# Kernel optimization log

Hardware: AMD Instinct MI355X
Metric: run time of the kernel (lower is better)

## Reference

```python
import jax, jax.numpy as jnp
import numpy as np

K = 4096            # ca3_memory_slots
C = 2048            # ca3_code_dim
B = 8192            # query batch (episodes)
MAX_ITERS = 8       # cfg.pseudoinverse_iterations (spiking window T=8)
TOL = 1e-4          # cfg.convergence_tolerance
ALPHA_CLAMP = 5e-4  # torch.clamp(exp(log_scale), max=5e-4)


def setup_inputs() -> dict:
    key = jax.random.key(0)
    k1, k2, k3 = jax.random.split(key, 3)
    query = jax.random.normal(k1, (B, C), dtype=jnp.float32)
    # buffer init: torch.randn(K, C) * 0.01
    memory_mean = jax.random.normal(k2, (K, C), dtype=jnp.float32) * 0.01
    # nn.Parameter(torch.tensor(pseudoinverse_alpha_init)) -> scalar
    ben_israel_log_scale = jnp.float32(-0.5)
    return {"query": query, "memory_mean": memory_mean,
            "ben_israel_log_scale": ben_israel_log_scale}


def _ben_israel_pinv(A, log_scale):
    """Ben-Israel-Cohen iteration with masked early stopping (fixed trip count)."""
    A_fro_sq = jnp.sum(A * A)
    alpha = (1.0 / (A_fro_sq + 1e-8)) * jnp.minimum(jnp.exp(log_scale), ALPHA_CLAMP)
    pinv = alpha * A.T                       # (C, K)
    residual = jnp.array(jnp.inf, dtype=A.dtype)
    done = jnp.array(False)
    for _ in range(MAX_ITERS):
        pinv_new = 2.0 * pinv - pinv @ (A @ pinv)        # (C,K)
        recon = A @ (pinv_new @ A)                       # (K,C)
        res_new = jnp.linalg.norm(recon - A)             # Frobenius
        pinv = jnp.where(done, pinv, pinv_new)
        residual = jnp.where(done, residual, res_new)
        done = done | (res_new < TOL)
    return pinv, residual


def reference(query, memory_mean, ben_israel_log_scale):
    A = memory_mean                                      # (K, C)
    A_pinv, residual = _ben_israel_pinv(A, ben_israel_log_scale)  # (C, K)
    w = query @ A_pinv                                   # (B, K) addressing weights
    retrieved = w @ A                                    # (B, C) pattern completion
    return retrieved
```

## Files before the change

### kernel.cpp

```cpp
#include <hip/hip_runtime.h>
#include <hip/hip_bf16.h>
#include <cstdint>
#include <cstddef>


#define K_DIM 4096
#define C_DIM 2048
#define B_DIM 8192
#define SPLITK 4
#define KCHUNK (K_DIM / SPLITK)

typedef __bf16 bf16x8 __attribute__((ext_vector_type(8)));
typedef float f32x4 __attribute__((ext_vector_type(4)));

#define VMCNT(n) asm volatile("s_waitcnt vmcnt(" #n ")" ::: "memory")
#define LGKMCNT0 asm volatile("s_waitcnt lgkmcnt(0)" ::: "memory")
#define SBAR __builtin_amdgcn_s_barrier()

__device__ __forceinline__ void async_load16(const void* g, void* l) {
  __builtin_amdgcn_global_load_lds(
      (const __attribute__((address_space(1))) void*)g,
      (__attribute__((address_space(3))) void*)l, 16, 0, 0);
}

__global__ __launch_bounds__(256) void prep_kernel(
    const float* __restrict__ A, __hip_bfloat16* __restrict__ At,
    const float* __restrict__ q, __hip_bfloat16* __restrict__ qb,
    float* __restrict__ wsf) {
  const int b = blockIdx.x;
  const int t = threadIdx.x;
  if (b < 2048) {
    __shared__ __align__(16) __hip_bfloat16 Ts[64 * 68];
    const int c0 = (b & 31) * 64;
    const int k0 = (b >> 5) * 64;
    const int c_l = t & 63;
    const int kq = t >> 6;
#pragma unroll
    for (int i = 0; i < 4; ++i) {
      int k_l = i * 16 + kq * 4;
      union { __hip_bfloat16 h[4]; uint2 u; } pk;
#pragma unroll
      for (int j = 0; j < 4; ++j)
        pk.h[j] = __float2bfloat16(A[(size_t)(k0 + k_l + j) * C_DIM + c0 + c_l]);
      *(uint2*)(Ts + c_l * 68 + k_l) = pk.u;
    }
    __syncthreads();
    const int c = t >> 2;
    const int seg = t & 3;
    const __hip_bfloat16* src = Ts + c * 68 + seg * 16;
    union { uint2 d[2]; uint4 qv; } o0, o1;
    o0.d[0] = *(const uint2*)(src + 0);
    o0.d[1] = *(const uint2*)(src + 4);
    o1.d[0] = *(const uint2*)(src + 8);
    o1.d[1] = *(const uint2*)(src + 12);
    __hip_bfloat16* dst = At + (size_t)(c0 + c) * K_DIM + k0 + seg * 16;
    *(uint4*)(dst + 0) = o0.qv;
    *(uint4*)(dst + 8) = o1.qv;
  } else {
    if (b == 2048 && t == 0) wsf[4] = 0.0f;
    const int n4 = B_DIM * C_DIM / 4;
    int tid = (b - 2048) * 256 + t;
    for (int i = tid; i < n4; i += 1024 * 256) {
      float4 v = ((const float4*)q)[i];
      __hip_bfloat16 o[4] = {__float2bfloat16(v.x), __float2bfloat16(v.y),
                             __float2bfloat16(v.z), __float2bfloat16(v.w)};
      *(uint2*)(qb + 4 * (size_t)i) = *(const uint2*)o;
    }
  }
}

__global__ __launch_bounds__(256, 4) void gemm_m(
    const __hip_bfloat16* __restrict__ At, float* __restrict__ P) {
  constexpr int BK = 64;
  constexpr int NT = KCHUNK / BK;
  __shared__ __align__(16) __hip_bfloat16 As[128 * BK];
  __shared__ __align__(16) __hip_bfloat16 Bs[128 * BK];
  const int bid = blockIdx.x;
  const int sw = (bid & 7) * 128 + (bid >> 3);
  const int z = sw >> 8;
  const int r = sw & 255;
  const int tn_i = r >> 4;
  const int tm_i = r & 15;
  const int tid = threadIdx.x;
  const int wave = tid >> 6, lane = tid & 63;
  const int tile_m = tm_i * 128, tile_n = tn_i * 128;
  const int kstart = z * KCHUNK;
  const int wm = (wave >> 1) * 64, wn = (wave & 1) * 64;
  const int lr = lane >> 3, lcl = (lane & 7) ^ lr;
  const __hip_bfloat16* aB =
      At + (size_t)(tile_m + wave * 32 + lr) * K_DIM + kstart + lcl * 8;
  const __hip_bfloat16* bB =
      At + (size_t)(tile_n + wave * 32 + lr) * K_DIM + kstart + lcl * 8;
  const int l15 = lane & 15, lg = lane >> 4, l7 = lane & 7;
  f32x4 acc[4][4] = {};

  for (int t = 0; t < NT; ++t) {
#pragma unroll
    for (int c = 0; c < 4; ++c) {
      async_load16(aB + (size_t)(c * 8) * K_DIM + (size_t)t * BK,
                   &As[(wave * 32 + c * 8) * BK]);
      async_load16(bB + (size_t)(c * 8) * K_DIM + (size_t)t * BK,
                   &Bs[(wave * 32 + c * 8) * BK]);
    }
    __syncthreads();
#pragma unroll
    for (int kh = 0; kh < 2; ++kh) {
      bf16x8 a[4], bb[4];
#pragma unroll
      for (int f = 0; f < 4; ++f) {
        a[f]  = *(const bf16x8*)&As[(wm + f * 16 + l15) * BK +
                                    (((kh * 4 + lg) ^ l7) * 8)];
        bb[f] = *(const bf16x8*)&Bs[(wn + f * 16 + l15) * BK +
                                    (((kh * 4 + lg) ^ l7) * 8)];
      }
      __builtin_amdgcn_s_setprio(1);
#pragma unroll
      for (int f = 0; f < 4; ++f)
#pragma unroll
        for (int j = 0; j < 4; ++j)
          acc[f][j] = __builtin_amdgcn_mfma_f32_16x16x32_bf16(
              a[f], bb[j], acc[f][j], 0, 0, 0);
      __builtin_amdgcn_s_setprio(0);
    }
    __syncthreads();
  }

  float* Pz = P + (size_t)z * C_DIM * C_DIM;
#pragma unroll
  for (int f = 0; f < 4; ++f) {
    const int gm = tile_m + wm + f * 16 + lg * 4;
#pragma unroll
    for (int j = 0; j < 4; ++j) {
      const int gn = tile_n + wn + j * 16 + l15;
#pragma unroll
      for (int r2 = 0; r2 < 4; ++r2)
        Pz[(size_t)(gm + r2) * C_DIM + gn] = acc[f][j][r2];
    }
  }
}

__global__ __launch_bounds__(256) void reduce4_kernel(
    const float* __restrict__ P, __hip_bfloat16* __restrict__ Mb,
    float* __restrict__ wsf) {
  const size_t CC = (size_t)C_DIM * C_DIM;
  const int n4 = (int)(CC / 4);
  int tid = blockIdx.x * blockDim.x + threadIdx.x;
  int stride = gridDim.x * blockDim.x;
  float tsum = 0.0f;
  bool hit = false;
  for (int i = tid; i < n4; i += stride) {
    float4 a = ((const float4*)P)[i];
#pragma unroll
    for (int z = 1; z < SPLITK; ++z) {
      float4 b = *(const float4*)(P + z * CC + (size_t)i * 4);
      a.x += b.x; a.y += b.y; a.z += b.z; a.w += b.w;
    }
    __hip_bfloat16 o[4] = {__float2bfloat16(a.x), __float2bfloat16(a.y),
                           __float2bfloat16(a.z), __float2bfloat16(a.w)};
    *(uint2*)(Mb + 4 * (size_t)i) = *(const uint2*)o;
    const int e0 = 4 * i;
    const int g = e0 >> 11;
    const int d = g * (C_DIM + 1);
    if (d >= e0 && d < e0 + 4) {
      const float av[4] = {a.x, a.y, a.z, a.w};
      tsum += av[d - e0];
      hit = true;
    }
  }
  if (hit) atomicAdd(wsf + 4, tsum);
}

__global__ __launch_bounds__(512, 2) void gemm_qm(
    const __hip_bfloat16* __restrict__ Ab, const __hip_bfloat16* __restrict__ Bb,
    float* __restrict__ Fp, const float* __restrict__ ls,
    const float* __restrict__ wsf) {
  constexpr int BK = 64;
  constexpr int NT = C_DIM / BK;
  __shared__ __align__(16) __hip_bfloat16 As[2][256 * BK];
  __shared__ __align__(16) __hip_bfloat16 Bs[2][256 * BK];
  const int bid = blockIdx.x;
  const int sw = (bid & 7) * 32 + (bid >> 3);
  const int tn_i = sw & 7;
  const int tm_i = sw >> 3;
  const int tid = threadIdx.x;
  const int wave = tid >> 6, lane = tid & 63;
  const int tile_m = tm_i * 256, tile_n = tn_i * 256;
  const int wm = (wave >> 2) * 128, wn = (wave & 3) * 64;
  const int lr = lane >> 3, lcl = (lane & 7) ^ lr;
  const __hip_bfloat16* aBase =
      Ab + (size_t)(tile_m + wave * 16 + lr) * C_DIM + lcl * 8;
  const __hip_bfloat16* bBase =
      Bb + (size_t)(tile_n + wave * 16 + lr) * C_DIM + lcl * 8;
  const int l15 = lane & 15, lg = lane >> 4, l7 = lane & 7;

  auto stA = [&](int buf, int h, int t) {
    const __hip_bfloat16* s = aBase + (size_t)(h * 128) * C_DIM + (size_t)t * BK;
    __hip_bfloat16* d = &As[buf][(h * 128 + wave * 16) * BK];
    async_load16(s, d);
    async_load16(s + (size_t)8 * C_DIM, d + 8 * BK);
  };
  auto stB = [&](int buf, int h, int t) {
    const __hip_bfloat16* s = bBase + (size_t)(h * 128) * C_DIM + (size_t)t * BK;
    __hip_bfloat16* d = &Bs[buf][(h * 128 + wave * 16) * BK];
    async_load16(s, d);
    async_load16(s + (size_t)8 * C_DIM, d + 8 * BK);
  };

  f32x4 acc[8][4] = {};

  stA(0, 0, 0); stA(0, 1, 0);
  stB(0, 0, 0); stB(0, 1, 0);
  stB(1, 0, 1); stB(1, 1, 1);
  VMCNT(4);
  SBAR;

  for (int t = 0; t < NT; ++t) {
    const int buf = t & 1;
    bf16x8 breg[4][2];
#pragma unroll
    for (int q = 0; q < 4; ++q) {
      bf16x8 af[2][2];
#pragma unroll
      for (int f = 0; f < 2; ++f)
#pragma unroll
        for (int s = 0; s < 2; ++s)
          af[f][s] = *(const bf16x8*)&As[buf][(wm + q * 32 + f * 16 + l15) * BK +
                                             ((((s << 2) | lg) ^ l7) << 3)];
      if (q == 0) {
#pragma unroll
        for (int j = 0; j < 4; ++j)
#pragma unroll
          for (int s = 0; s < 2; ++s)
            breg[j][s] = *(const bf16x8*)&Bs[buf][(wn + j * 16 + l15) * BK +
                                                 ((((s << 2) | lg) ^ l7) << 3)];
      }
      if (q == 0 && t + 1 < NT) stA(buf ^ 1, 0, t + 1);
      if (q == 1 && t + 1 < NT) stA(buf ^ 1, 1, t + 1);
      if (q == 2 && t + 2 < NT) stB(buf, 0, t + 2);
      if (q == 3) {
        if (t + 2 < NT) {
          stB(buf, 1, t + 2);
          VMCNT(4);
        } else {
          VMCNT(0);
        }
      }
      SBAR;
      LGKMCNT0;
      __builtin_amdgcn_s_setprio(1);
#pragma unroll
      for (int s = 0; s < 2; ++s)
#pragma unroll
        for (int f = 0; f < 2; ++f)
#pragma unroll
          for (int j = 0; j < 4; ++j)
            acc[q * 2 + f][j] = __builtin_amdgcn_mfma_f32_16x16x32_bf16(
                af[f][s], breg[j][s], acc[q * 2 + f][j], 0, 0, 0);
      __builtin_amdgcn_s_setprio(0);
      SBAR;
    }
  }

  const float c1 = 256.0f * fminf(expf(ls[0]), 5e-4f) / (wsf[4] + 1e-8f);
#pragma unroll
  for (int m = 0; m < 8; ++m) {
    const int gm = tile_m + wm + m * 16 + lg * 4;
#pragma unroll
    for (int j = 0; j < 4; ++j) {
      const int gn = tile_n + wn + j * 16 + l15;
#pragma unroll
      for (int r = 0; r < 4; ++r)
        Fp[(size_t)(gm + r) * C_DIM + gn] = c1 * acc[m][j][r];
    }
  }
}

extern "C" void kernel_launch(void* const* d_in, const int* in_sizes, int n_in,
                              void* d_out, int out_size, void* d_ws, size_t ws_size,
                              hipStream_t stream) {
  const float* query = (const float*)d_in[0];
  const float* A = (const float*)d_in[1];
  const float* ls = (const float*)d_in[2];
  float* out = (float*)d_out;

  char* ws = (char*)d_ws;
  float* wsf = (float*)ws;
  size_t off = 256;
  __hip_bfloat16* At = (__hip_bfloat16*)(ws + off);
  off += (size_t)C_DIM * K_DIM * 2;
  __hip_bfloat16* qb = (__hip_bfloat16*)(ws + off);
  off += (size_t)B_DIM * C_DIM * 2;
  __hip_bfloat16* Mb = (__hip_bfloat16*)(ws + off);

  float* P = out;

  prep_kernel<<<3072, 256, 0, stream>>>(A, At, query, qb, wsf);
  gemm_m<<<1024, 256, 0, stream>>>(At, P);
  reduce4_kernel<<<1024, 256, 0, stream>>>(P, Mb, wsf);
  gemm_qm<<<256, 512, 0, stream>>>(qb, Mb, out, ls, wsf);
}
```

Measured before the change: 275.3 us.

## Exploit symmetry of A^T A in split-K gram GEMM and restage gemm_qm pipeline

```diff
diff --git a/kernel.cpp b/kernel.cpp
--- a/kernel.cpp
+++ b/kernel.cpp
@@ -2,6 +2,7 @@
 #include <hip/hip_bf16.h>
 #include <cstdint>
 #include <cstddef>
+#include <math.h>
 
 
 #define K_DIM 4096
@@ -76,11 +77,14 @@
   __shared__ __align__(16) __hip_bfloat16 As[128 * BK];
   __shared__ __align__(16) __hip_bfloat16 Bs[128 * BK];
   const int bid = blockIdx.x;
-  const int sw = (bid & 7) * 128 + (bid >> 3);
-  const int z = sw >> 8;
-  const int r = sw & 255;
-  const int tn_i = r >> 4;
-  const int tm_i = r & 15;
+  const int sw = (bid & 7) * 68 + (bid >> 3);
+  const int z = sw / 136;
+  const int bt = sw % 136;
+  int r = (int)((sqrtf(8.0f * (float)bt + 1.0f) - 1.0f) * 0.5f);
+  if ((r + 1) * (r + 2) / 2 <= bt) ++r;
+  if (r * (r + 1) / 2 > bt) --r;
+  const int tm_i = r;
+  const int tn_i = bt - r * (r + 1) / 2;
   const int tid = threadIdx.x;
   const int wave = tid >> 6, lane = tid & 63;
   const int tile_m = tm_i * 128, tile_n = tn_i * 128;
@@ -126,6 +130,7 @@
   }
 
   float* Pz = P + (size_t)z * C_DIM * C_DIM;
+  const bool mirror = (tm_i != tn_i);
 #pragma unroll
   for (int f = 0; f < 4; ++f) {
     const int gm = tile_m + wm + f * 16 + lg * 4;
@@ -135,6 +140,10 @@
 #pragma unroll
       for (int r2 = 0; r2 < 4; ++r2)
         Pz[(size_t)(gm + r2) * C_DIM + gn] = acc[f][j][r2];
+      if (mirror) {
+        f32x4 v = acc[f][j];
+        *(f32x4*)&Pz[(size_t)gn * C_DIM + gm] = v;
+      }
     }
   }
 }
@@ -207,6 +216,30 @@
   };
 
   f32x4 acc[8][4] = {};
+  bf16x8 af[4], bfr[4];
+
+  auto rdA = [&](int buf, int mh, int s) {
+#pragma unroll
+    for (int f = 0; f < 4; ++f)
+      af[f] = *(const bf16x8*)&As[buf][(wm + mh * 64 + f * 16 + l15) * BK +
+                                       (((s * 4 + lg) ^ l7) * 8)];
+  };
+  auto rdB = [&](int buf, int s) {
+#pragma unroll
+    for (int j = 0; j < 4; ++j)
+      bfr[j] = *(const bf16x8*)&Bs[buf][(wn + j * 16 + l15) * BK +
+                                        (((s * 4 + lg) ^ l7) * 8)];
+  };
+  auto mm = [&](int mh) {
+    __builtin_amdgcn_s_setprio(1);
+#pragma unroll
+    for (int f = 0; f < 4; ++f)
+#pragma unroll
+      for (int j = 0; j < 4; ++j)
+        acc[mh * 4 + f][j] = __builtin_amdgcn_mfma_f32_16x16x32_bf16(
+            af[f], bfr[j], acc[mh * 4 + f][j], 0, 0, 0);
+    __builtin_amdgcn_s_setprio(0);
+  };
 
   stA(0, 0, 0); stA(0, 1, 0);
   stB(0, 0, 0); stB(0, 1, 0);
@@ -216,49 +249,28 @@
 
   for (int t = 0; t < NT; ++t) {
     const int buf = t & 1;
-    bf16x8 breg[4][2];
-#pragma unroll
-    for (int q = 0; q < 4; ++q) {
-      bf16x8 af[2][2];
-#pragma unroll
-      for (int f = 0; f < 2; ++f)
-#pragma unroll
-        for (int s = 0; s < 2; ++s)
-          af[f][s] = *(const bf16x8*)&As[buf][(wm + q * 32 + f * 16 + l15) * BK +
-                                             ((((s << 2) | lg) ^ l7) << 3)];
-      if (q == 0) {
-#pragma unroll
-        for (int j = 0; j < 4; ++j)
-#pragma unroll
-          for (int s = 0; s < 2; ++s)
-            breg[j][s] = *(const bf16x8*)&Bs[buf][(wn + j * 16 + l15) * BK +
-                                                 ((((s << 2) | lg) ^ l7) << 3)];
-      }
-      if (q == 0 && t + 1 < NT) stA(buf ^ 1, 0, t + 1);
-      if (q == 1 && t + 1 < NT) stA(buf ^ 1, 1, t + 1);
-      if (q == 2 && t + 2 < NT) stB(buf, 0, t + 2);
-      if (q == 3) {
-        if (t + 2 < NT) {
-          stB(buf, 1, t + 2);
-          VMCNT(4);
-        } else {
-          VMCNT(0);
-        }
-      }
-      SBAR;
-      LGKMCNT0;
-      __builtin_amdgcn_s_setprio(1);
-#pragma unroll
-      for (int s = 0; s < 2; ++s)
-#pragma unroll
-        for (int f = 0; f < 2; ++f)
-#pragma unroll
-          for (int j = 0; j < 4; ++j)
-            acc[q * 2 + f][j] = __builtin_amdgcn_mfma_f32_16x16x32_bf16(
-                af[f][s], breg[j][s], acc[q * 2 + f][j], 0, 0, 0);
-      __builtin_amdgcn_s_setprio(0);
-      SBAR;
-    }
+    rdA(buf, 0, 0);
+    rdB(buf, 0);
+    SBAR;
+    if (t + 1 < NT) stA(buf ^ 1, 0, t + 1);
+    LGKMCNT0;
+    mm(0);
+    rdA(buf, 1, 0);
+    SBAR;
+    if (t + 1 < NT) stA(buf ^ 1, 1, t + 1);
+    LGKMCNT0;
+    mm(1);
+    rdA(buf, 0, 1);
+    rdB(buf, 1);
+    SBAR;
+    LGKMCNT0;
+    mm(0);
+    rdA(buf, 1, 1);
+    VMCNT(0);
+    SBAR;
+    if (t + 2 < NT) { stB(buf, 0, t + 2); stB(buf, 1, t + 2); }
+    LGKMCNT0;
+    mm(1);
   }
 
   const float c1 = 256.0f * fminf(expf(ls[0]), 5e-4f) / (wsf[4] + 1e-8f);
@@ -295,7 +307,7 @@
   float* P = out;
 
   prep_kernel<<<3072, 256, 0, stream>>>(A, At, query, qb, wsf);
-  gemm_m<<<1024, 256, 0, stream>>>(At, P);
+  gemm_m<<<544, 256, 0, stream>>>(At, P);
   reduce4_kernel<<<1024, 256, 0, stream>>>(P, Mb, wsf);
   gemm_qm<<<256, 512, 0, stream>>>(qb, Mb, out, ls, wsf);
 }
```

After: 270.5 us. About the same (-1.8%).
